# Performance work log

Measured on AMD Instinct MI355X. Metric: run time of the kernel, lower is better.

Reference implementation:

```python
import jax, jax.numpy as jnp
import numpy as np

N_USER = 100000
N_ITEM = 50000
N = N_USER + N_ITEM
E = 1000000
D = 64
B = 4096
GAMMA = -0.45
ZETA = 1.05
LAMBDA0 = 1e-4
REG_WEIGHT = 1e-4


def setup_inputs() -> dict:
    key = jax.random.key(0)
    ks = jax.random.split(key, 20)
    s = 1.0 / np.sqrt(D)
    inp = {
        'features': jax.random.normal(ks[0], (N, D), jnp.float32) * 0.1,
        'row': jax.random.randint(ks[1], (E,), 0, N, jnp.int32),
        'col': jax.random.randint(ks[2], (E,), 0, N, jnp.int32),
        'users': jax.random.randint(ks[3], (B,), 0, N_USER, jnp.int32),
        'items': jax.random.randint(ks[4], (B,), 0, N_ITEM, jnp.int32),
        'neg_items': jax.random.randint(ks[5], (B,), 0, N_ITEM, jnp.int32),
        'u0': jax.random.uniform(ks[6], (E, 1), jnp.float32, 1e-7, 1.0 - 1e-7),
        'u1': jax.random.uniform(ks[7], (E, 1), jnp.float32, 1e-7, 1.0 - 1e-7),
        'temperature': jnp.full((1,), 0.5, jnp.float32),
        'W_nb0': jax.random.normal(ks[8], (D, D), jnp.float32) * s,
        'b_nb0': jnp.zeros((D,), jnp.float32),
        'W_self0': jax.random.normal(ks[9], (D, D), jnp.float32) * s,
        'b_self0': jnp.zeros((D,), jnp.float32),
        'W_att0': jax.random.normal(ks[10], (2 * D, 1), jnp.float32) * s,
        'b_att0': jnp.zeros((1,), jnp.float32),
        'W_nb1': jax.random.normal(ks[11], (D, D), jnp.float32) * s,
        'b_nb1': jnp.zeros((D,), jnp.float32),
        'W_self1': jax.random.normal(ks[12], (D, D), jnp.float32) * s,
        'b_self1': jnp.zeros((D,), jnp.float32),
        'W_att1': jax.random.normal(ks[13], (2 * D, 1), jnp.float32) * s,
        'b_att1': jnp.zeros((1,), jnp.float32),
    }
    return inp


def _edge_layer(x, row, col, u, Wn, bn, Ws, bs, Wa, ba, temp):
    # edge-gather attention MLP: [E, D] gathers + small GEMMs
    h_nb = jax.nn.relu(x[row] @ Wn + bn)
    h_self = jax.nn.relu(x[col] @ Ws + bs)
    log_alpha = jnp.concatenate([h_nb, h_self], axis=1) @ Wa + ba  # [E, 1]
    # hard-concrete sample (training=True): logistic noise + stretch + clip
    noise = jnp.log(u) - jnp.log1p(-u)
    gate = jax.nn.sigmoid((noise + log_alpha) / temp)
    mask = jnp.clip(gate * (ZETA - GAMMA) + GAMMA, 0.0, 1.0)[:, 0]  # [E]
    # sparse symmetric degree normalization
    rowsum = jax.ops.segment_sum(mask, row, num_segments=N) + 1e-6
    d_inv_sqrt = jnp.clip(rowsum ** -0.5, 0.0, 10.0)
    vals = mask * d_inv_sqrt[row] * d_inv_sqrt[col]
    # SpMM: x_next[r] = sum_e vals[e] * x[col[e]]
    x_next = jax.ops.segment_sum(vals[:, None] * x[col], row, num_segments=N)
    return x_next, log_alpha


def reference(features, row, col, users, items, neg_items, u0, u1, temperature,
              W_nb0, b_nb0, W_self0, b_self0, W_att0, b_att0,
              W_nb1, b_nb1, W_self1, b_self1, W_att1, b_att1):
    t = temperature[0]
    x1, w0 = _edge_layer(features, row, col, u0, W_nb0, b_nb0, W_self0, b_self0, W_att0, b_att0, t)
    x2, w1 = _edge_layer(x1, row, col, u1, W_nb1, b_nb1, W_self1, b_self1, W_att1, b_att1, t)
    xs = features + x1 + x2  # sum(embedsLst)
    x_user, x_item = xs[:N_USER], xs[N_USER:]
    anc, pos, neg = x_user[users], x_item[items], x_item[neg_items]
    pos_scores = jnp.sum(anc * pos, axis=1)
    neg_scores = jnp.sum(anc * neg, axis=1)
    bpr = -jnp.mean(jnp.log(jax.nn.sigmoid(pos_scores - neg_scores) + 1e-5))
    params = [W_nb0, b_nb0, W_self0, b_self0, W_att0, b_att0,
              W_nb1, b_nb1, W_self1, b_self1, W_att1, b_att1]
    reg = sum(jnp.sum(p * p) for p in params) * REG_WEIGHT
    lt = jnp.log(-GAMMA / ZETA)
    l0 = (jnp.mean(jax.nn.sigmoid(w0 - t * lt)) + jnp.mean(jax.nn.sigmoid(w1 - t * lt))) * LAMBDA0
    return bpr + reg + l0
```

## Files before the change

kernel.cpp:

```cpp
#include <hip/hip_runtime.h>
#include <hip/hip_bf16.h>

#define N_TOT   150000
#define N_USER  100000
#define E_TOT   1000000
#define B_TOT   4096
#define D_DIM   64

#define NSCAN_PAD   150016
#define BKT_SHIFT   10
#define BKT_ROWS    (1 << BKT_SHIFT)
#define NBKT        ((N_TOT + BKT_ROWS - 1) / BKT_ROWS)
#define BKT_CAP     8192
#define BIN_CHUNK   4096
#define NBIN_BLOCKS ((E_TOT + BIN_CHUNK - 1) / BIN_CHUNK)
#define COL_MASK    0x3FFFF

typedef short short8v  __attribute__((ext_vector_type(8)));
typedef float float4v  __attribute__((ext_vector_type(4)));

__device__ __forceinline__ float b2f(unsigned int lo16)
{
    union { unsigned int u; float f; } c; c.u = lo16 << 16; return c.f;
}
__device__ __forceinline__ unsigned short f2b(float f)
{
    union { float f; unsigned int u; } c; c.f = f;
    unsigned int u = c.u + 0x7FFFu + ((c.u >> 16) & 1u);
    return (unsigned short)(u >> 16);
}
__device__ __forceinline__ unsigned short f2h(float f)
{
    union { _Float16 h; unsigned short u; } c; c.h = (_Float16)f; return c.u;
}
__device__ __forceinline__ float h2f(unsigned short u)
{
    union { unsigned short u; _Float16 h; } c; c.u = u; return (float)c.h;
}
__device__ __forceinline__ int   f_as_i(float f) { union { float f; int i; } c; c.f = f; return c.i; }
__device__ __forceinline__ float i_as_f(int i)   { union { int i; float f; } c; c.i = i; return c.f; }

__global__ void prep_kernel(const float4* __restrict__ in, ushort4* __restrict__ out, int n4,
                            const float* __restrict__ Wn0, const float* __restrict__ Ws0,
                            const float* __restrict__ Wn1, const float* __restrict__ Ws1,
                            unsigned short* __restrict__ wpk)
{
    if (blockIdx.x < 1024) {
        for (int i = blockIdx.x * 256 + threadIdx.x; i < n4; i += 1024 * 256) {
            float4 v = in[i];
            ushort4 o;
            o.x = f2b(v.x); o.y = f2b(v.y); o.z = f2b(v.z); o.w = f2b(v.w);
            out[i] = o;
        }
        return;
    }
    int f = (blockIdx.x - 1024) * 256 + threadIdx.x;
    if (f >= 2048) return;
    const float* W[4] = {Wn0, Ws0, Wn1, Ws1};
    int m   = f >> 9;
    int rem = f & 511;
    int kb  = rem >> 8;
    int nt  = (rem >> 6) & 3;
    int l   = rem & 63;
    const float* Wm = W[m];
    int kbase = 32 * kb + ((l >> 4) << 3);
    int n     = 16 * nt + (l & 15);
    unsigned short o[8];
    #pragma unroll
    for (int j = 0; j < 8; ++j) o[j] = f2b(Wm[(kbase + j) * 64 + n]);
    ushort4* dst = (ushort4*)(wpk + (size_t)f * 8);
    dst[0] = make_ushort4(o[0], o[1], o[2], o[3]);
    dst[1] = make_ushort4(o[4], o[5], o[6], o[7]);
}

__global__ __launch_bounds__(256)
void node_scalars_mfma_kernel(const unsigned short* __restrict__ xb,
                              const unsigned short* __restrict__ wpack,
                              const float* __restrict__ bn, const float* __restrict__ bs,
                              const float* __restrict__ Wa,
                              float* __restrict__ a_nb, float* __restrict__ a_self,
                              int nNodes)
{
    const int lane = threadIdx.x & 63;
    const int wid  = (blockIdx.x * blockDim.x + threadIdx.x) >> 6;
    const int nodeBase = wid * 16;
    if (nodeBase >= nNodes) return;

    short8v bfrag[2][2][4];
    #pragma unroll
    for (int m = 0; m < 2; ++m)
        #pragma unroll
        for (int kb = 0; kb < 2; ++kb)
            #pragma unroll
            for (int nt = 0; nt < 4; ++nt)
                bfrag[m][kb][nt] =
                    *(const short8v*)(wpack + (size_t)((((m * 2 + kb) * 4 + nt) * 64 + lane)) * 8);

    const size_t rowOff = (size_t)(nodeBase + (lane & 15)) * 64 + ((lane >> 4) << 3);
    short8v a0 = *(const short8v*)(xb + rowOff);
    short8v a1 = *(const short8v*)(xb + rowOff + 32);

    float4v acc[2][4];
    #pragma unroll
    for (int m = 0; m < 2; ++m)
        #pragma unroll
        for (int nt = 0; nt < 4; ++nt) {
            float4v z = {0.f, 0.f, 0.f, 0.f};
            z = __builtin_amdgcn_mfma_f32_16x16x32_bf16(a0, bfrag[m][0][nt], z, 0, 0, 0);
            z = __builtin_amdgcn_mfma_f32_16x16x32_bf16(a1, bfrag[m][1][nt], z, 0, 0, 0);
            acc[m][nt] = z;
        }

    const int j = lane & 15;
    float pn[4] = {0.f, 0.f, 0.f, 0.f};
    float ps[4] = {0.f, 0.f, 0.f, 0.f};
    #pragma unroll
    for (int nt = 0; nt < 4; ++nt) {
        float bnv = bn[nt * 16 + j], bsv = bs[nt * 16 + j];
        float wan = Wa[nt * 16 + j], was = Wa[64 + nt * 16 + j];
        #pragma unroll
        for (int r = 0; r < 4; ++r) {
            pn[r] = fmaf(fmaxf(acc[0][nt][r] + bnv, 0.f), wan, pn[r]);
            ps[r] = fmaf(fmaxf(acc[1][nt][r] + bsv, 0.f), was, ps[r]);
        }
    }
    #pragma unroll
    for (int off = 1; off < 16; off <<= 1) {
        #pragma unroll
        for (int r = 0; r < 4; ++r) {
            pn[r] += __shfl_xor(pn[r], off);
            ps[r] += __shfl_xor(ps[r], off);
        }
    }
    if (j == 0) {
        const int g = lane >> 4;
        #pragma unroll
        for (int r = 0; r < 4; ++r) {
            int node = nodeBase + g * 4 + r;
            a_nb[node]   = pn[r];
            a_self[node] = ps[r];
        }
    }
}

__global__ __launch_bounds__(256)
void bin_kernel(const int* __restrict__ row, const int* __restrict__ col,
                const float* __restrict__ u0, const float* __restrict__ u1,
                int* __restrict__ bcnt, int2* __restrict__ tmp, int nE)
{
    __shared__ int cnt[NBKT];
    __shared__ int base[NBKT];
    for (int i = threadIdx.x; i < NBKT; i += 256) cnt[i] = 0;
    __syncthreads();

    const int e0 = blockIdx.x * BIN_CHUNK + threadIdx.x;
    int r[16], w0[16], pk[16];
    #pragma unroll
    for (int k = 0; k < 16; ++k) {
        int e = e0 + k * 256;
        r[k] = (e < nE) ? row[e] : -1;
        if (r[k] >= 0) {
            int rl = r[k] & (BKT_ROWS - 1);
            w0[k] = (rl << 18) | col[e];
            float ua = u0[e], ub = u1[e];
            float n0 = __logf(__fdividef(ua, 1.0f - ua));
            float n1 = __logf(__fdividef(ub, 1.0f - ub));
            pk[k] = (int)(((unsigned int)f2h(n1) << 16) | (unsigned int)f2h(n0));
            atomicAdd(&cnt[r[k] >> BKT_SHIFT], 1);
        }
    }
    __syncthreads();

    for (int i = threadIdx.x; i < NBKT; i += 256) {
        int cc = cnt[i];
        base[i] = cc ? atomicAdd(&bcnt[i], cc) : 0;
        cnt[i] = 0;
    }
    __syncthreads();

    #pragma unroll
    for (int k = 0; k < 16; ++k) {
        if (r[k] >= 0) {
            int b   = r[k] >> BKT_SHIFT;
            int loc = atomicAdd(&cnt[b], 1);
            tmp[(size_t)b * BKT_CAP + base[b] + loc] = make_int2(w0[k], pk[k]);
        }
    }
}

__global__ __launch_bounds__(256)
void scatter2_kernel(const int2* __restrict__ tmp, const int* __restrict__ bcnt,
                     int* __restrict__ start, int2* __restrict__ rec)
{
    __shared__ int pref[BKT_ROWS];
    __shared__ int wsum[256];
    __shared__ int sc[256];

    const int b     = blockIdx.x;
    const int rlo   = b << BKT_SHIFT;
    const int nrows = min(BKT_ROWS, N_TOT - rlo);
    const int t     = threadIdx.x;

    int v = (t < NBKT) ? bcnt[t] : 0;
    sc[t] = v;
    __syncthreads();
    for (int off = 1; off < 256; off <<= 1) {
        int x = sc[t];
        if (t >= off) x += sc[t - off];
        __syncthreads();
        sc[t] = x;
        __syncthreads();
    }
    const int cntb  = bcnt[b];
    const int baseb = (b == 0) ? 0 : sc[b - 1];
    if (b == 0 && t == 0) start[N_TOT] = E_TOT;

    const int2* __restrict__ bkt = tmp + (size_t)b * BKT_CAP;

    for (int i = t; i < BKT_ROWS; i += 256) pref[i] = 0;
    __syncthreads();

    for (int j = t; j < cntb; j += 256)
        atomicAdd(&pref[(unsigned int)bkt[j].x >> 18], 1);
    __syncthreads();

    const int base4 = t * 4;
    int v0 = pref[base4], v1 = pref[base4 + 1], v2 = pref[base4 + 2], v3 = pref[base4 + 3];
    int s = v0 + v1 + v2 + v3;
    wsum[t] = s;
    __syncthreads();
    for (int off = 1; off < 256; off <<= 1) {
        int x = wsum[t];
        if (t >= off) x += wsum[t - off];
        __syncthreads();
        wsum[t] = x;
        __syncthreads();
    }
    const int pre = wsum[t] - s;
    const int p0 = pre, p1 = pre + v0, p2 = pre + v0 + v1, p3 = pre + v0 + v1 + v2;

    if (base4     < nrows) start[rlo + base4]     = baseb + p0;
    if (base4 + 1 < nrows) start[rlo + base4 + 1] = baseb + p1;
    if (base4 + 2 < nrows) start[rlo + base4 + 2] = baseb + p2;
    if (base4 + 3 < nrows) start[rlo + base4 + 3] = baseb + p3;

    pref[base4] = p0; pref[base4 + 1] = p1; pref[base4 + 2] = p2; pref[base4 + 3] = p3;
    __syncthreads();

    for (int j = t; j < cntb; j += 256) {
        int2 q  = bkt[j];
        int loc = atomicAdd(&pref[(unsigned int)q.x >> 18], 1);
        rec[baseb + loc] = make_int2(q.x & COL_MASK, q.y);
    }
}

__global__ __launch_bounds__(256)
void edge_pass_a_kernel(const int2* __restrict__ rec, const int* __restrict__ start,
                        const int uSel,
                        const float* __restrict__ a_nb, const float* __restrict__ a_self,
                        const float* __restrict__ ba_p, const float* __restrict__ temp_p,
                        float2* __restrict__ wc, int2* __restrict__ range,
                        float* __restrict__ dis,
                        float* __restrict__ l0_accum, int nNodes)
{
    const float ba   = ba_p[0];
    const float t    = temp_p[0];
    const float invt = 1.0f / t;
    const float lt   = logf(0.45f / 1.05f);
    const float shift = t * lt;

    const int r = blockIdx.x * 256 + threadIdx.x;
    float l0local = 0.0f;

    if (r < nNodes) {
        const int js = start[r], je = start[r + 1];
        const float la_base = a_nb[r] + ba;
        float rs = 0.0f;
        int k = js;
        for (int j = js; j < je; ++j) {
            int2 q = rec[j];
            int c = q.x;
            float la = la_base + a_self[c];
            unsigned int pk = (unsigned int)q.y;
            float noise = h2f((unsigned short)(uSel ? (pk >> 16) : (pk & 0xFFFFu)));
            float gate  = 1.0f / (1.0f + __expf(-(noise + la) * invt));
            float m = fminf(fmaxf(gate * 1.5f - 0.45f, 0.0f), 1.0f);
            rs += m;
            l0local += 1.0f / (1.0f + __expf(-(la - shift)));
            if (m > 0.0f) { wc[k] = make_float2(m, i_as_f(c)); ++k; }
        }
        range[r] = make_int2(js, k);
        dis[r] = fminf(1.0f / sqrtf(rs + 1e-6f), 10.0f);
    }

    __shared__ float red[256];
    red[threadIdx.x] = l0local;
    __syncthreads();
    for (int s = 128; s > 0; s >>= 1) {
        if (threadIdx.x < s) red[threadIdx.x] += red[threadIdx.x + s];
        __syncthreads();
    }
    if (threadIdx.x == 0) unsafeAtomicAdd(l0_accum, red[0]);
}

__global__ void edge_gather_kernel(const float2* __restrict__ wc, const int2* __restrict__ range,
                                   const float* __restrict__ dis,
                                   const unsigned short* __restrict__ xb,
                                   unsigned short* __restrict__ xnb, int nNodes)
{
    const int lane = threadIdx.x & 63;
    const int oct  = lane >> 3;
    const int sub  = lane & 7;
    const int wave   = (blockIdx.x * blockDim.x + threadIdx.x) >> 6;
    const int nWaves = (gridDim.x * blockDim.x) >> 6;
    const int nOcts  = (nNodes + 7) >> 3;

    for (int p = wave; p < nOcts; p += nWaves) {
        const int r = 8 * p + oct;
        const bool valid = r < nNodes;
        const int rr = valid ? r : nNodes - 1;
        int2 rg  = range[rr];
        float dr = dis[rr];
        int j  = rg.x;
        int je = valid ? rg.y : rg.x;
        float a0 = 0.f, a1 = 0.f, a2 = 0.f, a3 = 0.f;
        float a4 = 0.f, a5 = 0.f, a6 = 0.f, a7 = 0.f;
        for (; j + 4 <= je; j += 4) {
            float2 w0 = wc[j], w1 = wc[j + 1], w2 = wc[j + 2], w3 = wc[j + 3];
            int c0 = f_as_i(w0.y), c1 = f_as_i(w1.y), c2 = f_as_i(w2.y), c3 = f_as_i(w3.y);
            float s0 = w0.x * dis[c0], s1 = w1.x * dis[c1];
            float s2 = w2.x * dis[c2], s3 = w3.x * dis[c3];
            uint4 q0 = *(const uint4*)(xb + (size_t)c0 * 64 + sub * 8);
            uint4 q1 = *(const uint4*)(xb + (size_t)c1 * 64 + sub * 8);
            uint4 q2 = *(const uint4*)(xb + (size_t)c2 * 64 + sub * 8);
            uint4 q3 = *(const uint4*)(xb + (size_t)c3 * 64 + sub * 8);
            a0 = fmaf(s0, b2f(q0.x & 0xFFFFu), a0); a1 = fmaf(s0, b2f(q0.x >> 16), a1);
            a2 = fmaf(s0, b2f(q0.y & 0xFFFFu), a2); a3 = fmaf(s0, b2f(q0.y >> 16), a3);
            a4 = fmaf(s0, b2f(q0.z & 0xFFFFu), a4); a5 = fmaf(s0, b2f(q0.z >> 16), a5);
            a6 = fmaf(s0, b2f(q0.w & 0xFFFFu), a6); a7 = fmaf(s0, b2f(q0.w >> 16), a7);
            a0 = fmaf(s1, b2f(q1.x & 0xFFFFu), a0); a1 = fmaf(s1, b2f(q1.x >> 16), a1);
            a2 = fmaf(s1, b2f(q1.y & 0xFFFFu), a2); a3 = fmaf(s1, b2f(q1.y >> 16), a3);
            a4 = fmaf(s1, b2f(q1.z & 0xFFFFu), a4); a5 = fmaf(s1, b2f(q1.z >> 16), a5);
            a6 = fmaf(s1, b2f(q1.w & 0xFFFFu), a6); a7 = fmaf(s1, b2f(q1.w >> 16), a7);
            a0 = fmaf(s2, b2f(q2.x & 0xFFFFu), a0); a1 = fmaf(s2, b2f(q2.x >> 16), a1);
            a2 = fmaf(s2, b2f(q2.y & 0xFFFFu), a2); a3 = fmaf(s2, b2f(q2.y >> 16), a3);
            a4 = fmaf(s2, b2f(q2.z & 0xFFFFu), a4); a5 = fmaf(s2, b2f(q2.z >> 16), a5);
            a6 = fmaf(s2, b2f(q2.w & 0xFFFFu), a6); a7 = fmaf(s2, b2f(q2.w >> 16), a7);
            a0 = fmaf(s3, b2f(q3.x & 0xFFFFu), a0); a1 = fmaf(s3, b2f(q3.x >> 16), a1);
            a2 = fmaf(s3, b2f(q3.y & 0xFFFFu), a2); a3 = fmaf(s3, b2f(q3.y >> 16), a3);
            a4 = fmaf(s3, b2f(q3.z & 0xFFFFu), a4); a5 = fmaf(s3, b2f(q3.z >> 16), a5);
            a6 = fmaf(s3, b2f(q3.w & 0xFFFFu), a6); a7 = fmaf(s3, b2f(q3.w >> 16), a7);
        }
        for (; j < je; ++j) {
            float2 w0 = wc[j];
            int c0 = f_as_i(w0.y);
            float s0 = w0.x * dis[c0];
            uint4 q0 = *(const uint4*)(xb + (size_t)c0 * 64 + sub * 8);
            a0 = fmaf(s0, b2f(q0.x & 0xFFFFu), a0); a1 = fmaf(s0, b2f(q0.x >> 16), a1);
            a2 = fmaf(s0, b2f(q0.y & 0xFFFFu), a2); a3 = fmaf(s0, b2f(q0.y >> 16), a3);
            a4 = fmaf(s0, b2f(q0.z & 0xFFFFu), a4); a5 = fmaf(s0, b2f(q0.z >> 16), a5);
            a6 = fmaf(s0, b2f(q0.w & 0xFFFFu), a6); a7 = fmaf(s0, b2f(q0.w >> 16), a7);
        }
        if (valid) {
            uint4 o;
            o.x = ((unsigned int)f2b(a1 * dr) << 16) | (unsigned int)f2b(a0 * dr);
            o.y = ((unsigned int)f2b(a3 * dr) << 16) | (unsigned int)f2b(a2 * dr);
            o.z = ((unsigned int)f2b(a5 * dr) << 16) | (unsigned int)f2b(a4 * dr);
            o.w = ((unsigned int)f2b(a7 * dr) << 16) | (unsigned int)f2b(a6 * dr);
            *(uint4*)(xnb + (size_t)r * 64 + sub * 8) = o;
        }
    }
}

__global__ void loss_kernel(const float* __restrict__ f,
                            const unsigned short* __restrict__ x1b,
                            const unsigned short* __restrict__ x2b,
                            const int* __restrict__ users, const int* __restrict__ items,
                            const int* __restrict__ negs,
                            const float* __restrict__ w0, const float* __restrict__ b0,
                            const float* __restrict__ w1, const float* __restrict__ b1,
                            const float* __restrict__ wa0, const float* __restrict__ ba0,
                            const float* __restrict__ w2, const float* __restrict__ b2,
                            const float* __restrict__ w3, const float* __restrict__ b3,
                            const float* __restrict__ wa1, const float* __restrict__ ba1,
                            float* __restrict__ scal, int B)
{
    const int t = threadIdx.x;
    if (blockIdx.x == 64) {
        float s = 0.0f;
        for (int i = t; i < 4096; i += 256)
            s += w0[i]*w0[i] + w1[i]*w1[i] + w2[i]*w2[i] + w3[i]*w3[i];
        for (int i = t; i < 64; i += 256)
            s += b0[i]*b0[i] + b1[i]*b1[i] + b2[i]*b2[i] + b3[i]*b3[i];
        for (int i = t; i < 128; i += 256)
            s += wa0[i]*wa0[i] + wa1[i]*wa1[i];
        if (t == 0) s += ba0[0]*ba0[0] + ba1[0]*ba1[0];

        __shared__ float red[256];
        red[t] = s;
        __syncthreads();
        for (int st = 128; st > 0; st >>= 1) {
            if (t < st) red[t] += red[t + st];
            __syncthreads();
        }
        if (t == 0) scal[1] = red[0];
        return;
    }

    const int lane   = t & 63;
    const int wave   = (blockIdx.x * 256 + t) >> 6;
    const int nWaves = (64 * 256) >> 6;

    float local = 0.0f;
    for (int b = wave; b < B; b += nWaves) {
        size_t ui = (size_t)users[b] * 64 + lane;
        size_t pi = (size_t)(N_USER + items[b]) * 64 + lane;
        size_t ni = (size_t)(N_USER + negs[b]) * 64 + lane;
        float a = f[ui] + b2f(x1b[ui]) + b2f(x2b[ui]);
        float p = f[pi] + b2f(x1b[pi]) + b2f(x2b[pi]);
        float n = f[ni] + b2f(x1b[ni]) + b2f(x2b[ni]);
        float ps = a * p, ns = a * n;
        #pragma unroll
        for (int off = 32; off; off >>= 1) {
            ps += __shfl_xor(ps, off);
            ns += __shfl_xor(ns, off);
        }
        if (lane == 0) {
            float s = 1.0f / (1.0f + expf(-(ps - ns)));
            local += -logf(s + 1e-5f);
        }
    }
    if (lane == 0) unsafeAtomicAdd(&scal[0], local);
}

__global__ void finalize_kernel(const float* __restrict__ scal, float* __restrict__ out)
{
    float bpr = scal[0] / (float)B_TOT;
    float reg = scal[1] * 1e-4f;
    float l0  = (scal[2] + scal[3]) * (1e-4f / (float)E_TOT);
    out[0] = bpr + reg + l0;
}

extern "C" void kernel_launch(void* const* d_in, const int* in_sizes, int n_in,
                              void* d_out, int out_size, void* d_ws, size_t ws_size,
                              hipStream_t stream)
{
    const float* features = (const float*)d_in[0];
    const int*   row      = (const int*)d_in[1];
    const int*   col      = (const int*)d_in[2];
    const int*   users    = (const int*)d_in[3];
    const int*   items    = (const int*)d_in[4];
    const int*   negs     = (const int*)d_in[5];
    const float* u0       = (const float*)d_in[6];
    const float* u1       = (const float*)d_in[7];
    const float* temp     = (const float*)d_in[8];
    const float* W_nb0    = (const float*)d_in[9];
    const float* b_nb0    = (const float*)d_in[10];
    const float* W_self0  = (const float*)d_in[11];
    const float* b_self0  = (const float*)d_in[12];
    const float* W_att0   = (const float*)d_in[13];
    const float* b_att0   = (const float*)d_in[14];
    const float* W_nb1    = (const float*)d_in[15];
    const float* b_nb1    = (const float*)d_in[16];
    const float* W_self1  = (const float*)d_in[17];
    const float* b_self1  = (const float*)d_in[18];
    const float* W_att1   = (const float*)d_in[19];
    const float* b_att1   = (const float*)d_in[20];
    float* out = (float*)d_out;

    float* ws = (float*)d_ws;
    unsigned short* fb  = (unsigned short*)ws;
    unsigned short* x1b = (unsigned short*)(ws + 4800000);
    unsigned short* x2b = (unsigned short*)(ws + 9600000);
    float* scal  = ws + 14400000;
    int*   bcnt  = (int*)(scal + 16);
    int*   start = bcnt + 160;
    int2*  tmp   = (int2*)(start + NSCAN_PAD);
    float2* wc   = (float2*)tmp;
    int2*  rec   = tmp + (size_t)NBKT * BKT_CAP;
    int2*  range = rec + E_TOT;
    float* dis   = (float*)(range + N_TOT);
    float* a_nb  = dis + N_TOT;
    float* a_self= a_nb + N_TOT;
    unsigned short* wpk =
        (unsigned short*)(((uintptr_t)(a_self + N_TOT) + 15) & ~(uintptr_t)15);

    hipMemsetAsync(scal, 0, (16 + 160) * sizeof(float), stream);

    const int nNodeBlocks = (N_TOT + 255) / 256;
    const int nMfmaBlocks = (N_TOT / 16 + 3) / 4;

    prep_kernel<<<1032, 256, 0, stream>>>((const float4*)features, (ushort4*)fb, N_TOT * 16,
                                          W_nb0, W_self0, W_nb1, W_self1, wpk);

    bin_kernel<<<NBIN_BLOCKS, 256, 0, stream>>>(row, col, u0, u1, bcnt, tmp, E_TOT);
    scatter2_kernel<<<NBKT, 256, 0, stream>>>(tmp, bcnt, start, rec);

    node_scalars_mfma_kernel<<<nMfmaBlocks, 256, 0, stream>>>(fb, wpk, b_nb0, b_self0, W_att0,
                                                              a_nb, a_self, N_TOT);
    edge_pass_a_kernel<<<nNodeBlocks, 256, 0, stream>>>(rec, start, 0, a_nb, a_self,
                                                        b_att0, temp, wc, range, dis,
                                                        &scal[2], N_TOT);
    edge_gather_kernel<<<2048, 256, 0, stream>>>(wc, range, dis, fb, x1b, N_TOT);

    node_scalars_mfma_kernel<<<nMfmaBlocks, 256, 0, stream>>>(x1b, wpk + 8192, b_nb1, b_self1,
                                                              W_att1, a_nb, a_self, N_TOT);
    edge_pass_a_kernel<<<nNodeBlocks, 256, 0, stream>>>(rec, start, 1, a_nb, a_self,
                                                        b_att1, temp, wc, range, dis,
                                                        &scal[3], N_TOT);
    edge_gather_kernel<<<2048, 256, 0, stream>>>(wc, range, dis, x1b, x2b, N_TOT);

    loss_kernel<<<65, 256, 0, stream>>>(features, x1b, x2b, users, items, negs,
                                        W_nb0, b_nb0, W_self0, b_self0, W_att0, b_att0,
                                        W_nb1, b_nb1, W_self1, b_self1, W_att1, b_att1,
                                        scal, B_TOT);
    finalize_kernel<<<1, 1, 0, stream>>>(scal, out);
}
```

Measured before the change: 184.7 us.

## Merge prep with binning and scatter with layer-0 node scalars into shared launches

```diff
diff --git a/kernel.cpp b/kernel.cpp
--- a/kernel.cpp
+++ b/kernel.cpp
@@ -16,6 +16,9 @@
 #define NBIN_BLOCKS ((E_TOT + BIN_CHUNK - 1) / BIN_CHUNK)
 #define COL_MASK    0x3FFFF
 
+#define PREP_BLKS   1032
+#define NS_BLKS     2344
+
 typedef short short8v  __attribute__((ext_vector_type(8)));
 typedef float float4v  __attribute__((ext_vector_type(4)));
 
@@ -40,49 +43,14 @@
 __device__ __forceinline__ int   f_as_i(float f) { union { float f; int i; } c; c.f = f; return c.i; }
 __device__ __forceinline__ float i_as_f(int i)   { union { int i; float f; } c; c.i = i; return c.f; }
 
-__global__ void prep_kernel(const float4* __restrict__ in, ushort4* __restrict__ out, int n4,
-                            const float* __restrict__ Wn0, const float* __restrict__ Ws0,
-                            const float* __restrict__ Wn1, const float* __restrict__ Ws1,
-                            unsigned short* __restrict__ wpk)
-{
-    if (blockIdx.x < 1024) {
-        for (int i = blockIdx.x * 256 + threadIdx.x; i < n4; i += 1024 * 256) {
-            float4 v = in[i];
-            ushort4 o;
-            o.x = f2b(v.x); o.y = f2b(v.y); o.z = f2b(v.z); o.w = f2b(v.w);
-            out[i] = o;
-        }
-        return;
-    }
-    int f = (blockIdx.x - 1024) * 256 + threadIdx.x;
-    if (f >= 2048) return;
-    const float* W[4] = {Wn0, Ws0, Wn1, Ws1};
-    int m   = f >> 9;
-    int rem = f & 511;
-    int kb  = rem >> 8;
-    int nt  = (rem >> 6) & 3;
-    int l   = rem & 63;
-    const float* Wm = W[m];
-    int kbase = 32 * kb + ((l >> 4) << 3);
-    int n     = 16 * nt + (l & 15);
-    unsigned short o[8];
-    #pragma unroll
-    for (int j = 0; j < 8; ++j) o[j] = f2b(Wm[(kbase + j) * 64 + n]);
-    ushort4* dst = (ushort4*)(wpk + (size_t)f * 8);
-    dst[0] = make_ushort4(o[0], o[1], o[2], o[3]);
-    dst[1] = make_ushort4(o[4], o[5], o[6], o[7]);
-}
-
-__global__ __launch_bounds__(256)
-void node_scalars_mfma_kernel(const unsigned short* __restrict__ xb,
-                              const unsigned short* __restrict__ wpack,
-                              const float* __restrict__ bn, const float* __restrict__ bs,
-                              const float* __restrict__ Wa,
-                              float* __restrict__ a_nb, float* __restrict__ a_self,
-                              int nNodes)
-{
-    const int lane = threadIdx.x & 63;
-    const int wid  = (blockIdx.x * blockDim.x + threadIdx.x) >> 6;
+__device__ __forceinline__
+void node_scalars_body(int wid, const unsigned short* __restrict__ xb,
+                       const unsigned short* __restrict__ wpack,
+                       const float* __restrict__ bn, const float* __restrict__ bs,
+                       const float* __restrict__ Wa,
+                       float* __restrict__ a_nb, float* __restrict__ a_self,
+                       int nNodes, int lane)
+{
     const int nodeBase = wid * 16;
     if (nodeBase >= nNodes) return;
 
@@ -144,16 +112,52 @@
 }
 
 __global__ __launch_bounds__(256)
-void bin_kernel(const int* __restrict__ row, const int* __restrict__ col,
-                const float* __restrict__ u0, const float* __restrict__ u1,
-                int* __restrict__ bcnt, int2* __restrict__ tmp, int nE)
+void prep_bin_kernel(const float4* __restrict__ in, ushort4* __restrict__ outb, int n4,
+                     const float* __restrict__ Wn0, const float* __restrict__ Ws0,
+                     const float* __restrict__ Wn1, const float* __restrict__ Ws1,
+                     unsigned short* __restrict__ wpk,
+                     const int* __restrict__ row, const int* __restrict__ col,
+                     const float* __restrict__ u0, const float* __restrict__ u1,
+                     int* __restrict__ bcnt, int2* __restrict__ tmp, int nE)
 {
     __shared__ int cnt[NBKT];
     __shared__ int base[NBKT];
+
+    if (blockIdx.x < 1024) {
+        for (int i = blockIdx.x * 256 + threadIdx.x; i < n4; i += 1024 * 256) {
+            float4 v = in[i];
+            ushort4 o;
+            o.x = f2b(v.x); o.y = f2b(v.y); o.z = f2b(v.z); o.w = f2b(v.w);
+            outb[i] = o;
+        }
+        return;
+    }
+    if (blockIdx.x < PREP_BLKS) {
+        int f = (blockIdx.x - 1024) * 256 + threadIdx.x;
+        if (f >= 2048) return;
+        const float* W[4] = {Wn0, Ws0, Wn1, Ws1};
+        int m   = f >> 9;
+        int rem = f & 511;
+        int kb  = rem >> 8;
+        int nt  = (rem >> 6) & 3;
+        int l   = rem & 63;
+        const float* Wm = W[m];
+        int kbase = 32 * kb + ((l >> 4) << 3);
+        int n     = 16 * nt + (l & 15);
+        unsigned short o[8];
+        #pragma unroll
+        for (int jj = 0; jj < 8; ++jj) o[jj] = f2b(Wm[(kbase + jj) * 64 + n]);
+        ushort4* dst = (ushort4*)(wpk + (size_t)f * 8);
+        dst[0] = make_ushort4(o[0], o[1], o[2], o[3]);
+        dst[1] = make_ushort4(o[4], o[5], o[6], o[7]);
+        return;
+    }
+
+    const int bb = blockIdx.x - PREP_BLKS;
     for (int i = threadIdx.x; i < NBKT; i += 256) cnt[i] = 0;
     __syncthreads();
 
-    const int e0 = blockIdx.x * BIN_CHUNK + threadIdx.x;
+    const int e0 = bb * BIN_CHUNK + threadIdx.x;
     int r[16], w0[16], pk[16];
     #pragma unroll
     for (int k = 0; k < 16; ++k) {
@@ -189,12 +193,24 @@
 }
 
 __global__ __launch_bounds__(256)
-void scatter2_kernel(const int2* __restrict__ tmp, const int* __restrict__ bcnt,
-                     int* __restrict__ start, int2* __restrict__ rec)
+void scatter_ns0_kernel(const int2* __restrict__ tmp, const int* __restrict__ bcnt,
+                        int* __restrict__ start, int2* __restrict__ rec,
+                        const unsigned short* __restrict__ fb,
+                        const unsigned short* __restrict__ wpk0,
+                        const float* __restrict__ bn, const float* __restrict__ bs,
+                        const float* __restrict__ Wa,
+                        float* __restrict__ a_nb, float* __restrict__ a_self)
 {
     __shared__ int pref[BKT_ROWS];
     __shared__ int wsum[256];
     __shared__ int sc[256];
+
+    if (blockIdx.x >= NBKT) {
+        const int lane = threadIdx.x & 63;
+        const int wid  = ((blockIdx.x - NBKT) * 256 + threadIdx.x) >> 6;
+        node_scalars_body(wid, fb, wpk0, bn, bs, Wa, a_nb, a_self, N_TOT, lane);
+        return;
+    }
 
     const int b     = blockIdx.x;
     const int rlo   = b << BKT_SHIFT;
@@ -252,6 +268,19 @@
         int loc = atomicAdd(&pref[(unsigned int)q.x >> 18], 1);
         rec[baseb + loc] = make_int2(q.x & COL_MASK, q.y);
     }
+}
+
+__global__ __launch_bounds__(256)
+void node_scalars_mfma_kernel(const unsigned short* __restrict__ xb,
+                              const unsigned short* __restrict__ wpack,
+                              const float* __restrict__ bn, const float* __restrict__ bs,
+                              const float* __restrict__ Wa,
+                              float* __restrict__ a_nb, float* __restrict__ a_self,
+                              int nNodes)
+{
+    const int lane = threadIdx.x & 63;
+    const int wid  = (blockIdx.x * blockDim.x + threadIdx.x) >> 6;
+    node_scalars_body(wid, xb, wpack, bn, bs, Wa, a_nb, a_self, nNodes, lane);
 }
 
 __global__ __launch_bounds__(256)
@@ -488,23 +517,22 @@
     hipMemsetAsync(scal, 0, (16 + 160) * sizeof(float), stream);
 
     const int nNodeBlocks = (N_TOT + 255) / 256;
-    const int nMfmaBlocks = (N_TOT / 16 + 3) / 4;
-
-    prep_kernel<<<1032, 256, 0, stream>>>((const float4*)features, (ushort4*)fb, N_TOT * 16,
-                                          W_nb0, W_self0, W_nb1, W_self1, wpk);
-
-    bin_kernel<<<NBIN_BLOCKS, 256, 0, stream>>>(row, col, u0, u1, bcnt, tmp, E_TOT);
-    scatter2_kernel<<<NBKT, 256, 0, stream>>>(tmp, bcnt, start, rec);
-
-    node_scalars_mfma_kernel<<<nMfmaBlocks, 256, 0, stream>>>(fb, wpk, b_nb0, b_self0, W_att0,
-                                                              a_nb, a_self, N_TOT);
+
+    prep_bin_kernel<<<PREP_BLKS + NBIN_BLOCKS, 256, 0, stream>>>(
+        (const float4*)features, (ushort4*)fb, N_TOT * 16,
+        W_nb0, W_self0, W_nb1, W_self1, wpk,
+        row, col, u0, u1, bcnt, tmp, E_TOT);
+
+    scatter_ns0_kernel<<<NBKT + NS_BLKS, 256, 0, stream>>>(
+        tmp, bcnt, start, rec, fb, wpk, b_nb0, b_self0, W_att0, a_nb, a_self);
+
     edge_pass_a_kernel<<<nNodeBlocks, 256, 0, stream>>>(rec, start, 0, a_nb, a_self,
                                                         b_att0, temp, wc, range, dis,
                                                         &scal[2], N_TOT);
     edge_gather_kernel<<<2048, 256, 0, stream>>>(wc, range, dis, fb, x1b, N_TOT);
 
-    node_scalars_mfma_kernel<<<nMfmaBlocks, 256, 0, stream>>>(x1b, wpk + 8192, b_nb1, b_self1,
-                                                              W_att1, a_nb, a_self, N_TOT);
+    node_scalars_mfma_kernel<<<NS_BLKS, 256, 0, stream>>>(x1b, wpk + 8192, b_nb1, b_self1,
+                                                          W_att1, a_nb, a_self, N_TOT);
     edge_pass_a_kernel<<<nNodeBlocks, 256, 0, stream>>>(rec, start, 1, a_nb, a_self,
                                                         b_att1, temp, wc, range, dis,
                                                         &scal[3], N_TOT);
```

Result: faster. 173.3 us (-6.1%).
